# Optimization experiments

Measured on AMD Instinct MI355X. Metric: run time of the kernel, lower is better.

Reference implementation:

```python
import jax, jax.numpy as jnp
import numpy as np

B, S, W, D = 64, 512, 400, 1024


def setup_inputs() -> dict:
    key = jax.random.key(0)
    k1, k2, k3 = jax.random.split(key, 3)
    bert_embedding = jax.random.normal(k1, (B, S, D), dtype=jnp.float32)
    # Non-overlapping sorted [st, ed) subword spans per batch row:
    # sort 2*W random boundaries in [0, S) and pair them up.
    bounds = jnp.sort(jax.random.randint(k2, (B, W * 2), 0, S), axis=1)
    x_bert_offset = bounds.reshape(B, W, 2).astype(jnp.int32)
    x_mask = jax.random.randint(k3, (B, W), 0, 2).astype(jnp.int32)
    return {
        "bert_embedding": bert_embedding,
        "x_bert_offset": x_bert_offset,
        "x_mask": x_mask,
    }


def reference(bert_embedding, x_bert_offset, x_mask):
    # bert_embedding: [B, S, D]; x_bert_offset: [B, W, 2]; x_mask: [B, W]
    st = x_bert_offset[..., 0]  # [B, W]
    ed = x_bert_offset[..., 1]  # [B, W]
    pos = jnp.arange(bert_embedding.shape[1])  # [S]
    # span membership mask: [B, W, S]
    span = (pos[None, None, :] >= st[..., None]) & (pos[None, None, :] < ed[..., None])
    span_f = span.astype(bert_embedding.dtype)
    # exact per-word subword sums via dense masked contraction
    sums = jnp.einsum("bws,bsd->bwd", span_f, bert_embedding)  # [B, W, D]
    lens = (ed - st).astype(bert_embedding.dtype)  # [B, W]
    valid = (x_mask != 0) & (ed > st)  # zero rows exactly as torch loop
    mean = sums / jnp.maximum(lens, 1.0)[..., None]
    out = jnp.where(valid[..., None], mean, 0.0)
    return out
```

## Files before the change

kernel.cpp:

```cpp
#include <hip/hip_runtime.h>
#include <hip/hip_bf16.h>

#define BB 64
#define SS 512
#define WW 400
#define DD 1024
#define D4 (DD / 4)

__global__ __launch_bounds__(256) void bert_span_mean(
    const float* __restrict__ emb,
    const int*   __restrict__ offs,
    const int*   __restrict__ mask,
    float*       __restrict__ out)
{
    const int bw = blockIdx.x;
    const int b  = bw / WW;

    const int st = offs[2 * bw];
    const int ed = offs[2 * bw + 1];
    const int m  = mask[bw];

    const int t = threadIdx.x;

    float4 acc = make_float4(0.f, 0.f, 0.f, 0.f);

    const bool valid = (m != 0) && (ed > st);
    if (valid) {
        const float4* src = reinterpret_cast<const float4*>(
            emb + (size_t)b * SS * DD) + t;
        for (int s = st; s < ed; ++s) {
            float4 v = src[(size_t)s * D4];
            acc.x += v.x; acc.y += v.y; acc.z += v.z; acc.w += v.w;
        }
        const float inv = 1.0f / (float)(ed - st);
        acc.x *= inv; acc.y *= inv; acc.z *= inv; acc.w *= inv;
    }

    reinterpret_cast<float4*>(out)[(size_t)bw * D4 + t] = acc;
}

extern "C" void kernel_launch(void* const* d_in, const int* in_sizes, int n_in,
                              void* d_out, int out_size, void* d_ws, size_t ws_size,
                              hipStream_t stream) {
    const float* emb  = (const float*)d_in[0];
    const int*   offs = (const int*)d_in[1];
    const int*   mask = (const int*)d_in[2];
    float*       out  = (float*)d_out;

    const int nblocks = BB * WW;
    bert_span_mean<<<nblocks, 256, 0, stream>>>(emb, offs, mask, out);
}
```

Measured before the change: 207.6 us.

## Use persistent wave-per-word kernel with prefetched offsets and nontemporal loads

Each wavefront now handles one word instead of each 256-thread block, and a fixed grid of 2048 blocks grid-strides over all words. Each lane loads four float4 chunks per row, rows are unrolled by two for more memory-level parallelism, and the next word's offsets and mask are prefetched. Loads and stores use nontemporal hints to reduce cache pollution. The risk is that nontemporal loads lose L2 reuse of embedding rows shared by nearby words, and a fixed grid may balance work poorly because span lengths vary.

```diff
diff --git a/kernel.cpp b/kernel.cpp
--- a/kernel.cpp
+++ b/kernel.cpp
@@ -1,11 +1,13 @@
 #include <hip/hip_runtime.h>
-#include <hip/hip_bf16.h>
 
 #define BB 64
 #define SS 512
 #define WW 400
 #define DD 1024
 #define D4 (DD / 4)
+#define NBW (BB * WW)
+
+typedef float f32x4 __attribute__((ext_vector_type(4)));
 
 __global__ __launch_bounds__(256) void bert_span_mean(
     const float* __restrict__ emb,
@@ -13,30 +15,76 @@
     const int*   __restrict__ mask,
     float*       __restrict__ out)
 {
-    const int bw = blockIdx.x;
-    const int b  = bw / WW;
+    const int lane = threadIdx.x & 63;
+    const int wid  = threadIdx.x >> 6;
+    const int nw   = gridDim.x << 2;
 
-    const int st = offs[2 * bw];
-    const int ed = offs[2 * bw + 1];
-    const int m  = mask[bw];
+    const int2* __restrict__ offs2 = reinterpret_cast<const int2*>(offs);
 
-    const int t = threadIdx.x;
+    int bw = (blockIdx.x << 2) + wid;
+    if (bw >= NBW) return;
 
-    float4 acc = make_float4(0.f, 0.f, 0.f, 0.f);
+    int2 se = offs2[bw];
+    int  m  = mask[bw];
 
-    const bool valid = (m != 0) && (ed > st);
-    if (valid) {
-        const float4* src = reinterpret_cast<const float4*>(
-            emb + (size_t)b * SS * DD) + t;
-        for (int s = st; s < ed; ++s) {
-            float4 v = src[(size_t)s * D4];
-            acc.x += v.x; acc.y += v.y; acc.z += v.z; acc.w += v.w;
+    while (true) {
+        const int bwn = bw + nw;
+        int2 sen = make_int2(0, 0);
+        int  mn  = 0;
+        if (bwn < NBW) {
+            sen = offs2[bwn];
+            mn  = mask[bwn];
         }
-        const float inv = 1.0f / (float)(ed - st);
-        acc.x *= inv; acc.y *= inv; acc.z *= inv; acc.w *= inv;
+
+        const int st = se.x;
+        const int ed = se.y;
+        const int b  = bw / WW;
+
+        f32x4 a0 = {0.f, 0.f, 0.f, 0.f};
+        f32x4 a1 = a0, a2 = a0, a3 = a0;
+
+        if (m != 0 && ed > st) {
+            const f32x4* __restrict__ src = reinterpret_cast<const f32x4*>(
+                emb + (size_t)b * (SS * DD)) + lane;
+            int s = st;
+            for (; s + 2 <= ed; s += 2) {
+                const f32x4* r0 = src + (size_t)s * D4;
+                const f32x4* r1 = r0 + D4;
+                f32x4 v0 = __builtin_nontemporal_load(r0);
+                f32x4 v1 = __builtin_nontemporal_load(r0 + 64);
+                f32x4 v2 = __builtin_nontemporal_load(r0 + 128);
+                f32x4 v3 = __builtin_nontemporal_load(r0 + 192);
+                f32x4 w0 = __builtin_nontemporal_load(r1);
+                f32x4 w1 = __builtin_nontemporal_load(r1 + 64);
+                f32x4 w2 = __builtin_nontemporal_load(r1 + 128);
+                f32x4 w3 = __builtin_nontemporal_load(r1 + 192);
+                a0 += v0; a1 += v1; a2 += v2; a3 += v3;
+                a0 += w0; a1 += w1; a2 += w2; a3 += w3;
+            }
+            if (s < ed) {
+                const f32x4* r0 = src + (size_t)s * D4;
+                f32x4 v0 = __builtin_nontemporal_load(r0);
+                f32x4 v1 = __builtin_nontemporal_load(r0 + 64);
+                f32x4 v2 = __builtin_nontemporal_load(r0 + 128);
+                f32x4 v3 = __builtin_nontemporal_load(r0 + 192);
+                a0 += v0; a1 += v1; a2 += v2; a3 += v3;
+            }
+            const float inv = 1.0f / (float)(ed - st);
+            a0 *= inv; a1 *= inv; a2 *= inv; a3 *= inv;
+        }
+
+        f32x4* __restrict__ dst =
+            reinterpret_cast<f32x4*>(out) + (size_t)bw * D4 + lane;
+        __builtin_nontemporal_store(a0, dst);
+        __builtin_nontemporal_store(a1, dst + 64);
+        __builtin_nontemporal_store(a2, dst + 128);
+        __builtin_nontemporal_store(a3, dst + 192);
+
+        if (bwn >= NBW) break;
+        bw = bwn;
+        se = sen;
+        m  = mn;
     }
-
-    reinterpret_cast<float4*>(out)[(size_t)bw * D4 + t] = acc;
 }
 
 extern "C" void kernel_launch(void* const* d_in, const int* in_sizes, int n_in,
@@ -47,6 +95,6 @@
     const int*   mask = (const int*)d_in[2];
     float*       out  = (float*)d_out;
 
-    const int nblocks = BB * WW;
+    const int nblocks = 2048;
     bert_span_mean<<<nblocks, 256, 0, stream>>>(emb, offs, mask, out);
 }
```

Result: faster. 202.9 us (-2.2%).
